# Performance work log

Measured on AMD Instinct MI355X. Metric: run time of the kernel, lower is better.

Reference implementation:

```python
import jax, jax.numpy as jnp
import numpy as np

B, T, C = 4, 2048, 1024
E, F, K = 8, 2048, 2


def setup_inputs() -> dict:
    key = jax.random.key(0)
    k0, k1, k2, k3 = jax.random.split(key, 4)
    s = lambda d: 1.0 / np.sqrt(d)
    x = jax.random.normal(k0, (B, T, C), dtype=jnp.float32)
    Wr = jax.random.normal(k1, (E, C), dtype=jnp.float32) * s(C)      # router: nn.Linear(C, E) weight [E, C]
    W1 = jax.random.normal(k2, (E, 2 * F, C), dtype=jnp.float32) * s(C)  # per-expert w1 [2F, C]
    W2 = jax.random.normal(k3, (E, C, F), dtype=jnp.float32) * s(F)      # per-expert w2 [C, F]
    return {"x": x, "Wr": Wr, "W1": W1, "W2": W2}


def reference(x, Wr, W1, W2):
    Bb, Tt, Cc = x.shape
    flat = x.reshape(-1, Cc)                         # [N, C]
    N = flat.shape[0]
    # router: top-k then softmax over the k selected logits
    logits = flat @ Wr.T                             # [N, E]
    weights, ids = jax.lax.top_k(logits, K)          # [N, K]
    weights = jax.nn.softmax(weights, axis=-1)
    rows = jnp.arange(N)[:, None]
    router_weights = jnp.zeros((N, E), dtype=flat.dtype).at[rows, ids].add(weights)  # [N, E]
    # all experts on all tokens (dense reference), SwiGLU
    h = jnp.einsum('nc,efc->nef', flat, W1)          # [N, E, 2F]
    val, gate = h[..., :F], h[..., F:]
    act = val * jax.nn.silu(gate)                    # [N, E, F]
    expert_outputs = jnp.einsum('nef,ecf->nec', act, W2)  # [N, E, C]
    out = jnp.einsum('nec,ne->nc', expert_outputs, router_weights)
    return out.reshape(Bb, Tt, Cc)
```

## Files before the change

### kernel.cpp

```cpp
#include <hip/hip_runtime.h>

#define NTOK 8192
#define CDIM 1024
#define FDIM 2048
#define NEXP 8
#define CAP  16384
#define NPAIR 16384
#define MTCAP 32

typedef __bf16 bf16x8 __attribute__((ext_vector_type(8)));
typedef float  f32x4  __attribute__((ext_vector_type(4)));

__device__ __forceinline__ unsigned short f2bf(float f) {
    unsigned int u = __builtin_bit_cast(unsigned int, f);
    unsigned int r = (u + 0x7FFFu + ((u >> 16) & 1u)) >> 16;
    return (unsigned short)r;
}

__device__ __forceinline__ unsigned int pack2(float lo, float hi) {
    return ((unsigned int)f2bf(hi) << 16) | (unsigned int)f2bf(lo);
}

__device__ __forceinline__ float bflo(unsigned int u) {
    return __builtin_bit_cast(float, u << 16);
}
__device__ __forceinline__ float bfhi(unsigned int u) {
    return __builtin_bit_cast(float, u & 0xFFFF0000u);
}

__device__ __forceinline__ void gload_lds16(const void* g, void* l) {
    __builtin_amdgcn_global_load_lds(
        (const __attribute__((address_space(1))) unsigned int*)g,
        (__attribute__((address_space(3))) unsigned int*)l, 16, 0, 0);
}

__global__ void cvt_kernel(const float* __restrict__ s, unsigned short* __restrict__ d, long ngrp) {
    long i = (long)blockIdx.x * blockDim.x + threadIdx.x;
    long stride = (long)gridDim.x * blockDim.x;
    const float4* s4 = (const float4*)s;
    uint4* d4 = (uint4*)d;
    for (long g = i; g < ngrp; g += stride) {
        float4 a = s4[2 * g], b = s4[2 * g + 1];
        uint4 o;
        o.x = pack2(a.x, a.y); o.y = pack2(a.z, a.w);
        o.z = pack2(b.x, b.y); o.w = pack2(b.z, b.w);
        d4[g] = o;
    }
}

__global__ __launch_bounds__(256) void logits_kernel(
    const float* __restrict__ x, const float* __restrict__ Wr,
    float* __restrict__ wgt, int* __restrict__ eids)
{
    int w = threadIdx.x >> 6, l = threadIdx.x & 63;
    int t = blockIdx.x * 4 + w;
    const float* xr = x + (size_t)t * CDIM;
    float acc[NEXP];
    #pragma unroll
    for (int e = 0; e < NEXP; e++) acc[e] = 0.f;
    for (int c = l; c < CDIM; c += 64) {
        float xv = xr[c];
        #pragma unroll
        for (int e = 0; e < NEXP; e++) acc[e] += xv * Wr[e * CDIM + c];
    }
    #pragma unroll
    for (int e = 0; e < NEXP; e++)
        for (int off = 32; off > 0; off >>= 1) acc[e] += __shfl_down(acc[e], off);
    if (l == 0) {
        int i0 = 0; float l0 = acc[0];
        #pragma unroll
        for (int e = 1; e < NEXP; e++) if (acc[e] > l0) { l0 = acc[e]; i0 = e; }
        int i1 = -1; float l1 = -3.4e38f;
        #pragma unroll
        for (int e = 0; e < NEXP; e++) if (e != i0 && acc[e] > l1) { l1 = acc[e]; i1 = e; }
        float tv = __expf(l1 - l0);
        float den = 1.f + tv;
        wgt[2 * t] = 1.f / den;
        wgt[2 * t + 1] = tv / den;
        eids[t] = i0 | (i1 << 8);
    }
}

__global__ __launch_bounds__(256) void bucket_kernel(
    const int* __restrict__ eids, int* __restrict__ list, int* __restrict__ cnt)
{
    __shared__ int lcnt[NEXP];
    __shared__ int lbase[NEXP];
    int t = threadIdx.x;
    if (t < NEXP) lcnt[t] = 0;
    __syncthreads();
    int tok = blockIdx.x * 256 + t;
    int id = eids[tok];
    int e0 = id & 0xff, e1 = (id >> 8) & 0xff;
    int s0 = atomicAdd(&lcnt[e0], 1);
    int s1 = atomicAdd(&lcnt[e1], 1);
    __syncthreads();
    if (t < NEXP) lbase[t] = atomicAdd(&cnt[t], lcnt[t]);
    __syncthreads();
    list[e0 * CAP + lbase[e0] + s0] = 2 * tok;
    list[e1 * CAP + lbase[e1] + s1] = 2 * tok + 1;
}

__global__ void offs_kernel(const int* __restrict__ cnt, int* __restrict__ offs) {
    if (threadIdx.x == 0) {
        int a = 0;
        for (int e = 0; e < NEXP; e++) { offs[e] = a; a += cnt[e]; }
    }
}

__global__ __launch_bounds__(256) void pack_kernel(
    const float* __restrict__ x, const int* __restrict__ list,
    const int* __restrict__ cnt, const int* __restrict__ offs,
    const float* __restrict__ wgt,
    unsigned short* __restrict__ xg, float* __restrict__ wgs)
{
    int e = blockIdx.y;
    int cnt_e = cnt[e];
    int s0 = blockIdx.x * 16;
    if (s0 >= cnt_e) return;
    int t = threadIdx.x;
    int sr = s0 + (t >> 4);
    if (sr >= cnt_e) return;
    int p = list[e * CAP + sr];
    int tok = p >> 1;
    if ((t & 15) == 0) wgs[offs[e] + sr] = wgt[p];
    const float4* src = (const float4*)(x + (size_t)tok * CDIM);
    uint2* dst = (uint2*)(xg + (size_t)(offs[e] + sr) * CDIM);
    int c = t & 15;
    #pragma unroll
    for (int i = 0; i < 16; i++) {
        float4 v = src[c + i * 16];
        uint2 o; o.x = pack2(v.x, v.y); o.y = pack2(v.z, v.w);
        dst[c + i * 16] = o;
    }
}

__global__ __launch_bounds__(256, 2) void gemm1_kernel(
    const unsigned short* __restrict__ xg,
    const unsigned short* __restrict__ W1b,
    const float* __restrict__ wgs,
    unsigned short* __restrict__ act,
    const int* __restrict__ cnt, const int* __restrict__ offs)
{
    int e = blockIdx.z, nt = blockIdx.x, mt = blockIdx.y;
    int cnt_e = cnt[e];
    if (mt * 128 >= cnt_e) return;
    int off_e = offs[e];

    __shared__ __align__(16) char lds[16384];

    int t = threadIdx.x, l = t & 63, w = t >> 6;
    int wave_m = w >> 1, wave_n = w & 1;

    int c2s = ((t & 3) * 16) ^ (((t >> 5) & 1) << 5);
    int dst = t * 16;

    const char *sA0, *sA1, *sBv, *sBg;
    {
        int r0 = min(mt * 128 + (t >> 2), cnt_e - 1);
        int r1 = min(mt * 128 + 64 + (t >> 2), cnt_e - 1);
        sA0 = (const char*)xg + (size_t)(off_e + r0) * 2048 + c2s;
        sA1 = (const char*)xg + (size_t)(off_e + r1) * 2048 + c2s;
        int f = nt * 64 + (t >> 2);
        sBv = (const char*)W1b + ((size_t)e * 2 * FDIM + f) * 2048 + c2s;
        sBg = sBv + (size_t)FDIM * 2048;
    }

    int lane_off = (l & 15) * 64 + (((l >> 4) * 16) ^ (((l >> 3) & 1) << 5));
    f32x4 accV[4][2] = {}, accG[4][2] = {};

    for (int kt = 0; kt < 32; kt++) {
        int kb = kt * 64;
        gload_lds16(sA0 + kb, (char*)lds + dst);
        gload_lds16(sA1 + kb, (char*)lds + 4096 + dst);
        gload_lds16(sBv + kb, (char*)lds + 8192 + dst);
        gload_lds16(sBg + kb, (char*)lds + 12288 + dst);
        __syncthreads();

        bf16x8 a0 = *(const bf16x8*)((char*)lds + (wave_m * 4 + 0) * 1024 + lane_off);
        bf16x8 a1 = *(const bf16x8*)((char*)lds + (wave_m * 4 + 1) * 1024 + lane_off);
        bf16x8 a2 = *(const bf16x8*)((char*)lds + (wave_m * 4 + 2) * 1024 + lane_off);
        bf16x8 a3 = *(const bf16x8*)((char*)lds + (wave_m * 4 + 3) * 1024 + lane_off);
        bf16x8 v0 = *(const bf16x8*)((char*)lds + 8192 + (wave_n * 2 + 0) * 1024 + lane_off);
        bf16x8 v1 = *(const bf16x8*)((char*)lds + 8192 + (wave_n * 2 + 1) * 1024 + lane_off);
        bf16x8 g0 = *(const bf16x8*)((char*)lds + 12288 + (wave_n * 2 + 0) * 1024 + lane_off);
        bf16x8 g1 = *(const bf16x8*)((char*)lds + 12288 + (wave_n * 2 + 1) * 1024 + lane_off);

        accV[0][0] = __builtin_amdgcn_mfma_f32_16x16x32_bf16(a0, v0, accV[0][0], 0, 0, 0);
        accV[0][1] = __builtin_amdgcn_mfma_f32_16x16x32_bf16(a0, v1, accV[0][1], 0, 0, 0);
        accG[0][0] = __builtin_amdgcn_mfma_f32_16x16x32_bf16(a0, g0, accG[0][0], 0, 0, 0);
        accG[0][1] = __builtin_amdgcn_mfma_f32_16x16x32_bf16(a0, g1, accG[0][1], 0, 0, 0);
        accV[1][0] = __builtin_amdgcn_mfma_f32_16x16x32_bf16(a1, v0, accV[1][0], 0, 0, 0);
        accV[1][1] = __builtin_amdgcn_mfma_f32_16x16x32_bf16(a1, v1, accV[1][1], 0, 0, 0);
        accG[1][0] = __builtin_amdgcn_mfma_f32_16x16x32_bf16(a1, g0, accG[1][0], 0, 0, 0);
        accG[1][1] = __builtin_amdgcn_mfma_f32_16x16x32_bf16(a1, g1, accG[1][1], 0, 0, 0);
        accV[2][0] = __builtin_amdgcn_mfma_f32_16x16x32_bf16(a2, v0, accV[2][0], 0, 0, 0);
        accV[2][1] = __builtin_amdgcn_mfma_f32_16x16x32_bf16(a2, v1, accV[2][1], 0, 0, 0);
        accG[2][0] = __builtin_amdgcn_mfma_f32_16x16x32_bf16(a2, g0, accG[2][0], 0, 0, 0);
        accG[2][1] = __builtin_amdgcn_mfma_f32_16x16x32_bf16(a2, g1, accG[2][1], 0, 0, 0);
        accV[3][0] = __builtin_amdgcn_mfma_f32_16x16x32_bf16(a3, v0, accV[3][0], 0, 0, 0);
        accV[3][1] = __builtin_amdgcn_mfma_f32_16x16x32_bf16(a3, v1, accV[3][1], 0, 0, 0);
        accG[3][0] = __builtin_amdgcn_mfma_f32_16x16x32_bf16(a3, g0, accG[3][0], 0, 0, 0);
        accG[3][1] = __builtin_amdgcn_mfma_f32_16x16x32_bf16(a3, g1, accG[3][1], 0, 0, 0);

        __syncthreads();
    }

    int colF = nt * 64 + wave_n * 32 + (l & 15);
    int rowB = mt * 128 + wave_m * 64 + ((l >> 4) * 4);
    #pragma unroll
    for (int m = 0; m < 4; m++) {
        #pragma unroll
        for (int r = 0; r < 4; r++) {
            int srow = rowB + m * 16 + r;
            if (srow < cnt_e) {
                float wsc = wgs[off_e + srow];
                #pragma unroll
                for (int n = 0; n < 2; n++) {
                    float g = accG[m][n][r];
                    float v = accV[m][n][r];
                    float aa = wsc * v * g / (1.f + __expf(-g));
                    act[(size_t)(off_e + srow) * FDIM + colF + n * 16] = f2bf(aa);
                }
            }
        }
    }
}

__global__ __launch_bounds__(256, 2) void gemm2_kernel(
    const unsigned short* __restrict__ act,
    const unsigned short* __restrict__ W2b,
    const int* __restrict__ list, const int* __restrict__ cnt,
    const int* __restrict__ offs,
    unsigned short* __restrict__ eob)
{
    int e = blockIdx.z, nt = blockIdx.x, mt = blockIdx.y;
    int cnt_e = cnt[e];
    if (mt * 128 >= cnt_e) return;
    int off_e = offs[e];
    const int* le = list + e * CAP;

    __shared__ __align__(16) char lds[16384];

    int t = threadIdx.x, l = t & 63, w = t >> 6;
    int wave_m = w >> 1, wave_n = w & 1;

    int c2s = ((t & 3) * 16) ^ (((t >> 5) & 1) << 5);
    int dst = t * 16;

    const char *sA0, *sA1, *sB0, *sB1;
    {
        int r0 = min(mt * 128 + (t >> 2), cnt_e - 1);
        int r1 = min(mt * 128 + 64 + (t >> 2), cnt_e - 1);
        sA0 = (const char*)act + (size_t)(off_e + r0) * 4096 + c2s;
        sA1 = (const char*)act + (size_t)(off_e + r1) * 4096 + c2s;
        int c0 = nt * 128 + (t >> 2);
        sB0 = (const char*)W2b + ((size_t)e * CDIM + c0) * 4096 + c2s;
        sB1 = sB0 + (size_t)64 * 4096;
    }

    int lane_off = (l & 15) * 64 + (((l >> 4) * 16) ^ (((l >> 3) & 1) << 5));
    f32x4 acc[4][4] = {};

    for (int kt = 0; kt < 64; kt++) {
        int kb = kt * 64;
        gload_lds16(sA0 + kb, (char*)lds + dst);
        gload_lds16(sA1 + kb, (char*)lds + 4096 + dst);
        gload_lds16(sB0 + kb, (char*)lds + 8192 + dst);
        gload_lds16(sB1 + kb, (char*)lds + 12288 + dst);
        __syncthreads();

        bf16x8 a0 = *(const bf16x8*)((char*)lds + (wave_m * 4 + 0) * 1024 + lane_off);
        bf16x8 a1 = *(const bf16x8*)((char*)lds + (wave_m * 4 + 1) * 1024 + lane_off);
        bf16x8 a2 = *(const bf16x8*)((char*)lds + (wave_m * 4 + 2) * 1024 + lane_off);
        bf16x8 a3 = *(const bf16x8*)((char*)lds + (wave_m * 4 + 3) * 1024 + lane_off);
        bf16x8 b0 = *(const bf16x8*)((char*)lds + 8192 + (wave_n * 4 + 0) * 1024 + lane_off);
        bf16x8 b1 = *(const bf16x8*)((char*)lds + 8192 + (wave_n * 4 + 1) * 1024 + lane_off);
        bf16x8 b2 = *(const bf16x8*)((char*)lds + 8192 + (wave_n * 4 + 2) * 1024 + lane_off);
        bf16x8 b3 = *(const bf16x8*)((char*)lds + 8192 + (wave_n * 4 + 3) * 1024 + lane_off);

        acc[0][0] = __builtin_amdgcn_mfma_f32_16x16x32_bf16(a0, b0, acc[0][0], 0, 0, 0);
        acc[0][1] = __builtin_amdgcn_mfma_f32_16x16x32_bf16(a0, b1, acc[0][1], 0, 0, 0);
        acc[0][2] = __builtin_amdgcn_mfma_f32_16x16x32_bf16(a0, b2, acc[0][2], 0, 0, 0);
        acc[0][3] = __builtin_amdgcn_mfma_f32_16x16x32_bf16(a0, b3, acc[0][3], 0, 0, 0);
        acc[1][0] = __builtin_amdgcn_mfma_f32_16x16x32_bf16(a1, b0, acc[1][0], 0, 0, 0);
        acc[1][1] = __builtin_amdgcn_mfma_f32_16x16x32_bf16(a1, b1, acc[1][1], 0, 0, 0);
        acc[1][2] = __builtin_amdgcn_mfma_f32_16x16x32_bf16(a1, b2, acc[1][2], 0, 0, 0);
        acc[1][3] = __builtin_amdgcn_mfma_f32_16x16x32_bf16(a1, b3, acc[1][3], 0, 0, 0);
        acc[2][0] = __builtin_amdgcn_mfma_f32_16x16x32_bf16(a2, b0, acc[2][0], 0, 0, 0);
        acc[2][1] = __builtin_amdgcn_mfma_f32_16x16x32_bf16(a2, b1, acc[2][1], 0, 0, 0);
        acc[2][2] = __builtin_amdgcn_mfma_f32_16x16x32_bf16(a2, b2, acc[2][2], 0, 0, 0);
        acc[2][3] = __builtin_amdgcn_mfma_f32_16x16x32_bf16(a2, b3, acc[2][3], 0, 0, 0);
        acc[3][0] = __builtin_amdgcn_mfma_f32_16x16x32_bf16(a3, b0, acc[3][0], 0, 0, 0);
        acc[3][1] = __builtin_amdgcn_mfma_f32_16x16x32_bf16(a3, b1, acc[3][1], 0, 0, 0);
        acc[3][2] = __builtin_amdgcn_mfma_f32_16x16x32_bf16(a3, b2, acc[3][2], 0, 0, 0);
        acc[3][3] = __builtin_amdgcn_mfma_f32_16x16x32_bf16(a3, b3, acc[3][3], 0, 0, 0);

        __syncthreads();
    }

    int colC = nt * 128 + wave_n * 64 + (l & 15);
    int rowB = mt * 128 + wave_m * 64 + ((l >> 4) * 4);
    #pragma unroll
    for (int m = 0; m < 4; m++) {
        #pragma unroll
        for (int r = 0; r < 4; r++) {
            int srow = rowB + m * 16 + r;
            if (srow < cnt_e) {
                int p = le[srow];
                #pragma unroll
                for (int n = 0; n < 4; n++)
                    eob[(size_t)p * CDIM + colC + n * 16] = f2bf(acc[m][n][r]);
            }
        }
    }
}

__global__ __launch_bounds__(256) void combine_kernel(
    const unsigned short* __restrict__ eob, float* __restrict__ out)
{
    const long NG = (long)NTOK * (CDIM / 4);
    long i = (long)blockIdx.x * blockDim.x + threadIdx.x;
    long stride = (long)gridDim.x * blockDim.x;
    float4* out4 = (float4*)out;
    for (long g = i; g < NG; g += stride) {
        long t = g >> 8;
        long j = g & 255;
        uint2 a = ((const uint2*)(eob + (size_t)(2 * t) * CDIM))[j];
        uint2 b = ((const uint2*)(eob + (size_t)(2 * t + 1) * CDIM))[j];
        float4 o;
        o.x = bflo(a.x) + bflo(b.x);
        o.y = bfhi(a.x) + bfhi(b.x);
        o.z = bflo(a.y) + bflo(b.y);
        o.w = bfhi(a.y) + bfhi(b.y);
        out4[g] = o;
    }
}

extern "C" void kernel_launch(void* const* d_in, const int* in_sizes, int n_in,
                              void* d_out, int out_size, void* d_ws, size_t ws_size,
                              hipStream_t stream) {
    const float* x  = (const float*)d_in[0];
    const float* Wr = (const float*)d_in[1];
    const float* W1 = (const float*)d_in[2];
    const float* W2 = (const float*)d_in[3];
    float* out = (float*)d_out;
    char* ws = (char*)d_ws;

    const size_t OFF_XG   = 0;
    const size_t OFF_W1B  = OFF_XG  + (size_t)NPAIR * CDIM * 2;
    const size_t OFF_ACT  = OFF_W1B + (size_t)NEXP * 2 * FDIM * CDIM * 2;
    const size_t OFF_LIST = OFF_ACT + (size_t)NPAIR * FDIM * 2;
    const size_t OFF_WGT  = OFF_LIST + (size_t)NEXP * CAP * 4;
    const size_t OFF_WGS  = OFF_WGT + (size_t)NPAIR * 4;
    const size_t OFF_CNT  = OFF_WGS + (size_t)NPAIR * 4;
    const size_t OFF_OFFS = OFF_CNT + 32;
    const size_t OFF_EIDS = OFF_OFFS + 32;

    unsigned short* xg  = (unsigned short*)(ws + OFF_XG);
    unsigned short* W1b = (unsigned short*)(ws + OFF_W1B);
    unsigned short* act = (unsigned short*)(ws + OFF_ACT);
    int*   list = (int*)(ws + OFF_LIST);
    float* wgt  = (float*)(ws + OFF_WGT);
    float* wgs  = (float*)(ws + OFF_WGS);
    int*   cnt  = (int*)(ws + OFF_CNT);
    int*   offs = (int*)(ws + OFF_OFFS);
    int*   eids = (int*)(ws + OFF_EIDS);
    unsigned short* W2b = (unsigned short*)(ws + OFF_W1B);
    unsigned short* eob = (unsigned short*)(ws + OFF_XG);

    hipMemsetAsync(cnt, 0, NEXP * sizeof(int), stream);

    cvt_kernel<<<4096, 256, 0, stream>>>(W1, W1b, (long)NEXP * 2 * FDIM * CDIM / 8);
    logits_kernel<<<NTOK / 4, 256, 0, stream>>>(x, Wr, wgt, eids);
    bucket_kernel<<<NTOK / 256, 256, 0, stream>>>(eids, list, cnt);
    offs_kernel<<<1, 64, 0, stream>>>(cnt, offs);
    pack_kernel<<<dim3(256, NEXP), 256, 0, stream>>>(x, list, cnt, offs, wgt, xg, wgs);

    gemm1_kernel<<<dim3(FDIM / 64, MTCAP, NEXP), 256, 0, stream>>>(xg, W1b, wgs, act, cnt, offs);

    cvt_kernel<<<4096, 256, 0, stream>>>(W2, W2b, (long)NEXP * CDIM * FDIM / 8);

    gemm2_kernel<<<dim3(CDIM / 128, MTCAP, NEXP), 256, 0, stream>>>(act, W2b, list, cnt, offs, eob);
    combine_kernel<<<2048, 256, 0, stream>>>(eob, out);
}
```

Before: 403.9 us.

## Prefetch next K tile during MFMA and double K step per iteration in expert GEMMs

```diff
diff --git a/kernel.cpp b/kernel.cpp
--- a/kernel.cpp
+++ b/kernel.cpp
@@ -33,6 +33,10 @@
         (const __attribute__((address_space(1))) unsigned int*)g,
         (__attribute__((address_space(3))) unsigned int*)l, 16, 0, 0);
 }
+
+#define BARRIER() asm volatile("s_barrier" ::: "memory")
+#define WAIT_LGKM0() do { asm volatile("s_waitcnt lgkmcnt(0)" ::: "memory"); __builtin_amdgcn_sched_barrier(0); } while (0)
+#define WAITVM0() asm volatile("s_waitcnt vmcnt(0)" ::: "memory")
 
 __global__ void cvt_kernel(const float* __restrict__ s, unsigned short* __restrict__ d, long ngrp) {
     long i = (long)blockIdx.x * blockDim.x + threadIdx.x;
@@ -147,7 +151,7 @@
     if (mt * 128 >= cnt_e) return;
     int off_e = offs[e];
 
-    __shared__ __align__(16) char lds[16384];
+    __shared__ __align__(16) char lds[32768];
 
     int t = threadIdx.x, l = t & 63, w = t >> 6;
     int wave_m = w >> 1, wave_n = w & 1;
@@ -169,42 +173,54 @@
     int lane_off = (l & 15) * 64 + (((l >> 4) * 16) ^ (((l >> 3) & 1) << 5));
     f32x4 accV[4][2] = {}, accG[4][2] = {};
 
-    for (int kt = 0; kt < 32; kt++) {
-        int kb = kt * 64;
-        gload_lds16(sA0 + kb, (char*)lds + dst);
-        gload_lds16(sA1 + kb, (char*)lds + 4096 + dst);
-        gload_lds16(sBv + kb, (char*)lds + 8192 + dst);
-        gload_lds16(sBg + kb, (char*)lds + 12288 + dst);
-        __syncthreads();
-
-        bf16x8 a0 = *(const bf16x8*)((char*)lds + (wave_m * 4 + 0) * 1024 + lane_off);
-        bf16x8 a1 = *(const bf16x8*)((char*)lds + (wave_m * 4 + 1) * 1024 + lane_off);
-        bf16x8 a2 = *(const bf16x8*)((char*)lds + (wave_m * 4 + 2) * 1024 + lane_off);
-        bf16x8 a3 = *(const bf16x8*)((char*)lds + (wave_m * 4 + 3) * 1024 + lane_off);
-        bf16x8 v0 = *(const bf16x8*)((char*)lds + 8192 + (wave_n * 2 + 0) * 1024 + lane_off);
-        bf16x8 v1 = *(const bf16x8*)((char*)lds + 8192 + (wave_n * 2 + 1) * 1024 + lane_off);
-        bf16x8 g0 = *(const bf16x8*)((char*)lds + 12288 + (wave_n * 2 + 0) * 1024 + lane_off);
-        bf16x8 g1 = *(const bf16x8*)((char*)lds + 12288 + (wave_n * 2 + 1) * 1024 + lane_off);
-
-        accV[0][0] = __builtin_amdgcn_mfma_f32_16x16x32_bf16(a0, v0, accV[0][0], 0, 0, 0);
-        accV[0][1] = __builtin_amdgcn_mfma_f32_16x16x32_bf16(a0, v1, accV[0][1], 0, 0, 0);
-        accG[0][0] = __builtin_amdgcn_mfma_f32_16x16x32_bf16(a0, g0, accG[0][0], 0, 0, 0);
-        accG[0][1] = __builtin_amdgcn_mfma_f32_16x16x32_bf16(a0, g1, accG[0][1], 0, 0, 0);
-        accV[1][0] = __builtin_amdgcn_mfma_f32_16x16x32_bf16(a1, v0, accV[1][0], 0, 0, 0);
-        accV[1][1] = __builtin_amdgcn_mfma_f32_16x16x32_bf16(a1, v1, accV[1][1], 0, 0, 0);
-        accG[1][0] = __builtin_amdgcn_mfma_f32_16x16x32_bf16(a1, g0, accG[1][0], 0, 0, 0);
-        accG[1][1] = __builtin_amdgcn_mfma_f32_16x16x32_bf16(a1, g1, accG[1][1], 0, 0, 0);
-        accV[2][0] = __builtin_amdgcn_mfma_f32_16x16x32_bf16(a2, v0, accV[2][0], 0, 0, 0);
-        accV[2][1] = __builtin_amdgcn_mfma_f32_16x16x32_bf16(a2, v1, accV[2][1], 0, 0, 0);
-        accG[2][0] = __builtin_amdgcn_mfma_f32_16x16x32_bf16(a2, g0, accG[2][0], 0, 0, 0);
-        accG[2][1] = __builtin_amdgcn_mfma_f32_16x16x32_bf16(a2, g1, accG[2][1], 0, 0, 0);
-        accV[3][0] = __builtin_amdgcn_mfma_f32_16x16x32_bf16(a3, v0, accV[3][0], 0, 0, 0);
-        accV[3][1] = __builtin_amdgcn_mfma_f32_16x16x32_bf16(a3, v1, accV[3][1], 0, 0, 0);
-        accG[3][0] = __builtin_amdgcn_mfma_f32_16x16x32_bf16(a3, g0, accG[3][0], 0, 0, 0);
-        accG[3][1] = __builtin_amdgcn_mfma_f32_16x16x32_bf16(a3, g1, accG[3][1], 0, 0, 0);
-
-        __syncthreads();
-    }
+#define G1_STAGE(KB) do { \
+        gload_lds16(sA0 + (KB),      (char*)lds + dst); \
+        gload_lds16(sA1 + (KB),      (char*)lds + 4096 + dst); \
+        gload_lds16(sA0 + (KB) + 64, (char*)lds + 8192 + dst); \
+        gload_lds16(sA1 + (KB) + 64, (char*)lds + 12288 + dst); \
+        gload_lds16(sBv + (KB),      (char*)lds + 16384 + dst); \
+        gload_lds16(sBv + (KB) + 64, (char*)lds + 20480 + dst); \
+        gload_lds16(sBg + (KB),      (char*)lds + 24576 + dst); \
+        gload_lds16(sBg + (KB) + 64, (char*)lds + 28672 + dst); \
+    } while (0)
+
+    G1_STAGE(0);
+
+    for (int kt = 0; kt < 16; kt++) {
+        WAITVM0();
+        BARRIER();
+
+        bf16x8 af[2][4], bv[2][2], bg[2][2];
+        #pragma unroll
+        for (int h = 0; h < 2; h++) {
+            #pragma unroll
+            for (int m = 0; m < 4; m++)
+                af[h][m] = *(const bf16x8*)((char*)lds + h * 8192 + (wave_m * 4 + m) * 1024 + lane_off);
+            #pragma unroll
+            for (int n = 0; n < 2; n++) {
+                bv[h][n] = *(const bf16x8*)((char*)lds + 16384 + h * 4096 + (wave_n * 2 + n) * 1024 + lane_off);
+                bg[h][n] = *(const bf16x8*)((char*)lds + 24576 + h * 4096 + (wave_n * 2 + n) * 1024 + lane_off);
+            }
+        }
+        WAIT_LGKM0();
+        BARRIER();
+
+        if (kt != 15) { int kb = (kt + 1) * 128; G1_STAGE(kb); }
+        __builtin_amdgcn_sched_barrier(0);
+
+        __builtin_amdgcn_s_setprio(1);
+        #pragma unroll
+        for (int h = 0; h < 2; h++)
+            #pragma unroll
+            for (int m = 0; m < 4; m++)
+                #pragma unroll
+                for (int n = 0; n < 2; n++) {
+                    accV[m][n] = __builtin_amdgcn_mfma_f32_16x16x32_bf16(af[h][m], bv[h][n], accV[m][n], 0, 0, 0);
+                    accG[m][n] = __builtin_amdgcn_mfma_f32_16x16x32_bf16(af[h][m], bg[h][n], accG[m][n], 0, 0, 0);
+                }
+        __builtin_amdgcn_s_setprio(0);
+    }
+#undef G1_STAGE
 
     int colF = nt * 64 + wave_n * 32 + (l & 15);
     int rowB = mt * 128 + wave_m * 64 + ((l >> 4) * 4);
@@ -240,7 +256,7 @@
     int off_e = offs[e];
     const int* le = list + e * CAP;
 
-    __shared__ __align__(16) char lds[16384];
+    __shared__ __align__(16) char lds[32768];
 
     int t = threadIdx.x, l = t & 63, w = t >> 6;
     int wave_m = w >> 1, wave_n = w & 1;
@@ -262,42 +278,50 @@
     int lane_off = (l & 15) * 64 + (((l >> 4) * 16) ^ (((l >> 3) & 1) << 5));
     f32x4 acc[4][4] = {};
 
-    for (int kt = 0; kt < 64; kt++) {
-        int kb = kt * 64;
-        gload_lds16(sA0 + kb, (char*)lds + dst);
-        gload_lds16(sA1 + kb, (char*)lds + 4096 + dst);
-        gload_lds16(sB0 + kb, (char*)lds + 8192 + dst);
-        gload_lds16(sB1 + kb, (char*)lds + 12288 + dst);
-        __syncthreads();
-
-        bf16x8 a0 = *(const bf16x8*)((char*)lds + (wave_m * 4 + 0) * 1024 + lane_off);
-        bf16x8 a1 = *(const bf16x8*)((char*)lds + (wave_m * 4 + 1) * 1024 + lane_off);
-        bf16x8 a2 = *(const bf16x8*)((char*)lds + (wave_m * 4 + 2) * 1024 + lane_off);
-        bf16x8 a3 = *(const bf16x8*)((char*)lds + (wave_m * 4 + 3) * 1024 + lane_off);
-        bf16x8 b0 = *(const bf16x8*)((char*)lds + 8192 + (wave_n * 4 + 0) * 1024 + lane_off);
-        bf16x8 b1 = *(const bf16x8*)((char*)lds + 8192 + (wave_n * 4 + 1) * 1024 + lane_off);
-        bf16x8 b2 = *(const bf16x8*)((char*)lds + 8192 + (wave_n * 4 + 2) * 1024 + lane_off);
-        bf16x8 b3 = *(const bf16x8*)((char*)lds + 8192 + (wave_n * 4 + 3) * 1024 + lane_off);
-
-        acc[0][0] = __builtin_amdgcn_mfma_f32_16x16x32_bf16(a0, b0, acc[0][0], 0, 0, 0);
-        acc[0][1] = __builtin_amdgcn_mfma_f32_16x16x32_bf16(a0, b1, acc[0][1], 0, 0, 0);
-        acc[0][2] = __builtin_amdgcn_mfma_f32_16x16x32_bf16(a0, b2, acc[0][2], 0, 0, 0);
-        acc[0][3] = __builtin_amdgcn_mfma_f32_16x16x32_bf16(a0, b3, acc[0][3], 0, 0, 0);
-        acc[1][0] = __builtin_amdgcn_mfma_f32_16x16x32_bf16(a1, b0, acc[1][0], 0, 0, 0);
-        acc[1][1] = __builtin_amdgcn_mfma_f32_16x16x32_bf16(a1, b1, acc[1][1], 0, 0, 0);
-        acc[1][2] = __builtin_amdgcn_mfma_f32_16x16x32_bf16(a1, b2, acc[1][2], 0, 0, 0);
-        acc[1][3] = __builtin_amdgcn_mfma_f32_16x16x32_bf16(a1, b3, acc[1][3], 0, 0, 0);
-        acc[2][0] = __builtin_amdgcn_mfma_f32_16x16x32_bf16(a2, b0, acc[2][0], 0, 0, 0);
-        acc[2][1] = __builtin_amdgcn_mfma_f32_16x16x32_bf16(a2, b1, acc[2][1], 0, 0, 0);
-        acc[2][2] = __builtin_amdgcn_mfma_f32_16x16x32_bf16(a2, b2, acc[2][2], 0, 0, 0);
-        acc[2][3] = __builtin_amdgcn_mfma_f32_16x16x32_bf16(a2, b3, acc[2][3], 0, 0, 0);
-        acc[3][0] = __builtin_amdgcn_mfma_f32_16x16x32_bf16(a3, b0, acc[3][0], 0, 0, 0);
-        acc[3][1] = __builtin_amdgcn_mfma_f32_16x16x32_bf16(a3, b1, acc[3][1], 0, 0, 0);
-        acc[3][2] = __builtin_amdgcn_mfma_f32_16x16x32_bf16(a3, b2, acc[3][2], 0, 0, 0);
-        acc[3][3] = __builtin_amdgcn_mfma_f32_16x16x32_bf16(a3, b3, acc[3][3], 0, 0, 0);
-
-        __syncthreads();
-    }
+#define G2_STAGE(KB) do { \
+        gload_lds16(sA0 + (KB),      (char*)lds + dst); \
+        gload_lds16(sA1 + (KB),      (char*)lds + 4096 + dst); \
+        gload_lds16(sA0 + (KB) + 64, (char*)lds + 8192 + dst); \
+        gload_lds16(sA1 + (KB) + 64, (char*)lds + 12288 + dst); \
+        gload_lds16(sB0 + (KB),      (char*)lds + 16384 + dst); \
+        gload_lds16(sB1 + (KB),      (char*)lds + 20480 + dst); \
+        gload_lds16(sB0 + (KB) + 64, (char*)lds + 24576 + dst); \
+        gload_lds16(sB1 + (KB) + 64, (char*)lds + 28672 + dst); \
+    } while (0)
+
+    G2_STAGE(0);
+
+    for (int kt = 0; kt < 32; kt++) {
+        WAITVM0();
+        BARRIER();
+
+        bf16x8 af[2][4], bf[2][4];
+        #pragma unroll
+        for (int h = 0; h < 2; h++) {
+            #pragma unroll
+            for (int m = 0; m < 4; m++)
+                af[h][m] = *(const bf16x8*)((char*)lds + h * 8192 + (wave_m * 4 + m) * 1024 + lane_off);
+            #pragma unroll
+            for (int n = 0; n < 4; n++)
+                bf[h][n] = *(const bf16x8*)((char*)lds + 16384 + h * 8192 + (wave_n * 4 + n) * 1024 + lane_off);
+        }
+        WAIT_LGKM0();
+        BARRIER();
+
+        if (kt != 31) { int kb = (kt + 1) * 128; G2_STAGE(kb); }
+        __builtin_amdgcn_sched_barrier(0);
+
+        __builtin_amdgcn_s_setprio(1);
+        #pragma unroll
+        for (int h = 0; h < 2; h++)
+            #pragma unroll
+            for (int m = 0; m < 4; m++)
+                #pragma unroll
+                for (int n = 0; n < 4; n++)
+                    acc[m][n] = __builtin_amdgcn_mfma_f32_16x16x32_bf16(af[h][m], bf[h][n], acc[m][n], 0, 0, 0);
+        __builtin_amdgcn_s_setprio(0);
+    }
+#undef G2_STAGE
 
     int colC = nt * 128 + wave_n * 64 + (l & 15);
     int rowB = mt * 128 + wave_m * 64 + ((l >> 4) * 4);
```

New measurement: 358.1 us. -11.4%, faster.
